# Performance work log

Hardware: AMD Instinct MI355X
Metric: run time of the kernel (lower is better)

The kernel has to match this reference:

```python
import jax, jax.numpy as jnp
import numpy as np

D_CLAMP = 10.0
FAPE_EPS = 1e-4
Z = 10.0
TORSION_EPS = 1e-8


def backbone_fape(R_pred, t_pred, x_pred, R_true, t_true, x_true):
    # R_*: [B,N,3,3], t_*/x_*: [B,N,3]
    Rp_inv = jnp.swapaxes(R_pred, -1, -2)
    tp_inv = -jnp.einsum('birc,bic->bir', Rp_inv, t_pred)
    Rt_inv = jnp.swapaxes(R_true, -1, -2)
    tt_inv = -jnp.einsum('birc,bic->bir', Rt_inv, t_true)
    # [B,N,N,3] local-frame coordinates
    xf_pred = jnp.einsum('biop,bjp->bijo', Rp_inv, x_pred) + tp_inv[:, :, None, :]
    xf_true = jnp.einsum('biop,bjp->bijo', Rt_inv, x_true) + tt_inv[:, :, None, :]
    dist = jnp.sqrt(jnp.sum((xf_pred - xf_true) ** 2, axis=-1) + FAPE_EPS)
    dist = jnp.minimum(dist, D_CLAMP)
    return jnp.mean(dist, axis=(-1, -2)) / Z  # [B]


def torsion_angle_loss(pred, true, true_alt):
    # pred/true/true_alt: [B,N,7,2]
    norm = jnp.sqrt(jnp.sum(pred ** 2, axis=-1, keepdims=True) + TORSION_EPS)
    pred_n = pred / norm
    d_true = jnp.sqrt(jnp.sum((true - pred_n) ** 2, axis=-1, keepdims=True) + TORSION_EPS)
    d_alt = jnp.sqrt(jnp.sum((true_alt - pred_n) ** 2, axis=-1, keepdims=True) + TORSION_EPS)
    torsion = jnp.mean(jnp.minimum(d_true, d_alt), axis=(2, 3))  # [B,N]
    angle_norm = jnp.mean(jnp.abs(norm - 1.0), axis=(2, 3))      # [B,N]
    return torsion + 0.02 * angle_norm


def setup_inputs() -> dict:
    key = jax.random.key(0)
    ks = jax.random.split(key, 7)
    L, B, N = 8, 2, 2048
    return {
        'traj_rotations': jax.random.normal(ks[0], (L, B, N, 3, 3), jnp.float32),
        'traj_translations': jax.random.normal(ks[1], (L, B, N, 3), jnp.float32),
        'traj_torsions': jax.random.normal(ks[2], (L, B, N, 7, 2), jnp.float32),
        'true_rotations': jax.random.normal(ks[3], (B, N, 3, 3), jnp.float32),
        'true_translations': jax.random.normal(ks[4], (B, N, 3), jnp.float32),
        'true_torsion_angles': jax.random.normal(ks[5], (B, N, 7, 2), jnp.float32),
        'true_torsion_angles_alt': jax.random.normal(ks[6], (B, N, 7, 2), jnp.float32),
    }


def reference(traj_rotations, traj_translations, traj_torsions,
              true_rotations, true_translations,
              true_torsion_angles, true_torsion_angles_alt):
    num_layers = traj_rotations.shape[0]
    total = jnp.zeros(traj_rotations.shape[1], traj_rotations.dtype)
    for l in range(num_layers):  # small fixed layer count
        fape = backbone_fape(traj_rotations[l], traj_translations[l], traj_translations[l],
                             true_rotations, true_translations, true_translations)
        torsion = torsion_angle_loss(traj_torsions[l], true_torsion_angles,
                                     true_torsion_angles_alt).mean(axis=-1)
        total = total + fape + torsion
    return total / num_layers
```

## Files before the change

kernel.cpp:

```cpp
#include <hip/hip_runtime.h>
#include <math.h>

constexpr int L = 8;
constexpr int B = 2;
constexpr int N = 2048;
constexpr int LB = L * B;
constexpr int ITEMS = LB * N;
constexpr int KF = 32;

constexpr float D_CLAMP2 = 100.0f;
constexpr float FAPE_EPS = 1e-4f;
constexpr float Z_CONST  = 10.0f;
constexpr float TEPS     = 1e-8f;

constexpr int THREADS = 256;
constexpr int JSPLIT  = 4;
constexpr int JCH     = N / JSPLIT;
constexpr int NPASS   = JCH / 128;
constexpr int NIT     = N / 64;
constexpr int FAPE_BLOCKS = LB * NIT * JSPLIT;
constexpr int TORS_PER_BLK = ITEMS / FAPE_BLOCKS;

typedef __attribute__((ext_vector_type(8))) short bf16x8;
typedef __attribute__((ext_vector_type(4))) float f32x4;

__device__ __forceinline__ float fast_sqrtf(float x) {
    return __builtin_amdgcn_sqrtf(x);
}
__device__ __forceinline__ unsigned short f2bf(float x) {
    unsigned u = __float_as_uint(x);
    u += 0x7fffu + ((u >> 16) & 1u);
    return (unsigned short)(u >> 16);
}
__device__ __forceinline__ float bf2f(unsigned short h) {
    return __uint_as_float((unsigned)h << 16);
}

__device__ __forceinline__ float wave_reduce_sum(float v) {
    #pragma unroll
    for (int off = 32; off > 0; off >>= 1)
        v += __shfl_down(v, off, 64);
    return v;
}

__device__ __forceinline__ float block_reduce_sum(float v) {
    __shared__ float s[4];
    v = wave_reduce_sum(v);
    int lane = threadIdx.x & 63;
    int w    = threadIdx.x >> 6;
    __syncthreads();
    if (lane == 0) s[w] = v;
    __syncthreads();
    return s[0] + s[1] + s[2] + s[3];
}

__device__ __forceinline__ void store_row(short* base, int r, const float* f) {
    #pragma unroll
    for (int c = 0; c < 4; ++c) {
        bf16x8 v;
        #pragma unroll
        for (int e = 0; e < 8; ++e) v[e] = (short)f2bf(f[8 * c + e]);
        const int p = c ^ ((r >> 1) & 3);
        *(bf16x8*)(base + r * KF + p * 8) = v;
    }
}
__device__ __forceinline__ bf16x8 load_frag(const short* base, int r, int c) {
    const int p = c ^ ((r >> 1) & 3);
    return *(const bf16x8*)(base + r * KF + p * 8);
}

__global__ __launch_bounds__(THREADS)
void fape_all_kernel(const float* __restrict__ traj_rot,
                     const float* __restrict__ traj_trans,
                     const float* __restrict__ traj_tors,
                     const float* __restrict__ true_rot,
                     const float* __restrict__ true_trans,
                     const float* __restrict__ t_true,
                     const float* __restrict__ t_alt,
                     float* __restrict__ partials)
{
    __shared__ short phiL[JCH * KF];
    __shared__ short psiL[64 * KF];
    __shared__ float tors_s;

    const int bid = blockIdx.x;
    const int jh  = bid & (JSPLIT - 1);
    const int it  = (bid >> 2) & (NIT - 1);
    const int lb  = bid >> 7;
    const int b   = lb & (B - 1);
    const int tid = threadIdx.x;

    const float* tp = traj_trans + (size_t)lb * N * 3;
    const float* tt = true_trans + (size_t)b  * N * 3;

    #pragma unroll
    for (int half = 0; half < 2; ++half) {
        const int r = tid + half * THREADS;
        const int j = jh * JCH + r;
        float u[6] = { tp[3 * j], tp[3 * j + 1], tp[3 * j + 2],
                       tt[3 * j], tt[3 * j + 1], tt[3 * j + 2] };
        float phi[KF];
        #pragma unroll
        for (int c = 0; c < 6; ++c) phi[c] = u[c] * u[c];
        int idx = 6;
        #pragma unroll
        for (int c = 0; c < 6; ++c)
            #pragma unroll
            for (int d = c + 1; d < 6; ++d)
                phi[idx++] = u[c] * u[d];
        #pragma unroll
        for (int c = 0; c < 6; ++c) phi[21 + c] = u[c];
        phi[27] = 1.0f;
        phi[28] = 1.0f;
        phi[29] = phi[30] = phi[31] = 0.0f;
        store_row(phiL, r, phi);
    }

    if (tid < 64) {
        const int r = tid;
        const int i = it * 64 + r;
        const float* Rp = traj_rot + ((size_t)lb * N + i) * 9;
        const float* Rt = true_rot + ((size_t)(b * N + i)) * 9;

        float W0[6], W1[6], W2[6];
        #pragma unroll
        for (int c = 0; c < 3; ++c) {
            W0[c] = Rp[3 * c];      W1[c] = Rp[3 * c + 1];      W2[c] = Rp[3 * c + 2];
            W0[c + 3] = -Rt[3 * c]; W1[c + 3] = -Rt[3 * c + 1]; W2[c + 3] = -Rt[3 * c + 2];
        }
        float u[6] = { tp[3 * i], tp[3 * i + 1], tp[3 * i + 2],
                       tt[3 * i], tt[3 * i + 1], tt[3 * i + 2] };

        float k0 = 0.f, k1 = 0.f, k2 = 0.f;
        #pragma unroll
        for (int c = 0; c < 6; ++c) {
            k0 = fmaf(W0[c], u[c], k0);
            k1 = fmaf(W1[c], u[c], k1);
            k2 = fmaf(W2[c], u[c], k2);
        }
        k0 = -k0; k1 = -k1; k2 = -k2;

        float psi[KF];
        #pragma unroll
        for (int c = 0; c < 6; ++c)
            psi[c] = fmaf(W0[c], W0[c], fmaf(W1[c], W1[c], W2[c] * W2[c]));
        int idx = 6;
        #pragma unroll
        for (int c = 0; c < 6; ++c)
            #pragma unroll
            for (int d = c + 1; d < 6; ++d)
                psi[idx++] = 2.0f * fmaf(W0[c], W0[d], fmaf(W1[c], W1[d], W2[c] * W2[d]));
        #pragma unroll
        for (int c = 0; c < 6; ++c)
            psi[21 + c] = 2.0f * fmaf(W0[c], k0, fmaf(W1[c], k1, W2[c] * k2));
        psi[27] = fmaf(k0, k0, fmaf(k1, k1, fmaf(k2, k2, FAPE_EPS)));
        psi[28] = psi[27] - bf2f(f2bf(psi[27]));
        psi[29] = psi[30] = psi[31] = 0.0f;
        store_row(psiL, r, psi);
    } else if (tid < 128) {
        const int t = tid - 64;
        float val = 0.0f;
        if (t < TORS_PER_BLK) {
            const int g  = bid * TORS_PER_BLK + t;
            const int n  = g & (N - 1);
            const int bn = b * N + n;
            const float* p  = traj_tors + (size_t)g * 14;
            const float* tr = t_true + (size_t)bn * 14;
            const float* al = t_alt  + (size_t)bn * 14;

            float st = 0.0f, sa = 0.0f;
            #pragma unroll
            for (int k = 0; k < 7; ++k) {
                const float px = p[2 * k], py = p[2 * k + 1];
                const float nrm = fast_sqrtf(fmaf(px, px, fmaf(py, py, TEPS)));
                const float inv = __builtin_amdgcn_rcpf(nrm);
                const float pnx = px * inv, pny = py * inv;
                const float tx = tr[2 * k] - pnx, ty = tr[2 * k + 1] - pny;
                const float ax = al[2 * k] - pnx, ay = al[2 * k + 1] - pny;
                const float dt = fast_sqrtf(fmaf(tx, tx, fmaf(ty, ty, TEPS)));
                const float da = fast_sqrtf(fmaf(ax, ax, fmaf(ay, ay, TEPS)));
                st += fminf(dt, da);
                sa += fabsf(nrm - 1.0f);
            }
            val = (st + 0.02f * sa) * (1.0f / 7.0f);
        }
        val = wave_reduce_sum(val);
        if (tid == 64) tors_s = val;
    }

    __syncthreads();

    const int w    = tid >> 6;
    const int lane = tid & 63;
    const int wm   = w >> 1;
    const int wn   = w & 1;
    const int r15  = lane & 15;
    const int cch  = lane >> 4;

    const bf16x8 a0 = load_frag(psiL, wm * 32 + r15, cch);
    const bf16x8 a1 = load_frag(psiL, wm * 32 + 16 + r15, cch);

    const f32x4 z = { 0.f, 0.f, 0.f, 0.f };
    float acc0 = 0.f, acc1 = 0.f, acc2 = 0.f, acc3 = 0.f;

    #pragma unroll
    for (int jp = 0; jp < NPASS; ++jp) {
        const int rb = jp * 128 + wn * 64 + r15;
        const bf16x8 b0 = load_frag(phiL, rb,      cch);
        const bf16x8 b1 = load_frag(phiL, rb + 16, cch);
        const bf16x8 b2 = load_frag(phiL, rb + 32, cch);
        const bf16x8 b3 = load_frag(phiL, rb + 48, cch);

        f32x4 d0 = __builtin_amdgcn_mfma_f32_16x16x32_bf16(a0, b0, z, 0, 0, 0);
        f32x4 d1 = __builtin_amdgcn_mfma_f32_16x16x32_bf16(a0, b1, z, 0, 0, 0);
        f32x4 d2 = __builtin_amdgcn_mfma_f32_16x16x32_bf16(a0, b2, z, 0, 0, 0);
        f32x4 d3 = __builtin_amdgcn_mfma_f32_16x16x32_bf16(a0, b3, z, 0, 0, 0);
        f32x4 d4 = __builtin_amdgcn_mfma_f32_16x16x32_bf16(a1, b0, z, 0, 0, 0);
        f32x4 d5 = __builtin_amdgcn_mfma_f32_16x16x32_bf16(a1, b1, z, 0, 0, 0);
        f32x4 d6 = __builtin_amdgcn_mfma_f32_16x16x32_bf16(a1, b2, z, 0, 0, 0);
        f32x4 d7 = __builtin_amdgcn_mfma_f32_16x16x32_bf16(a1, b3, z, 0, 0, 0);

        #pragma unroll
        for (int e = 0; e < 4; ++e) {
            acc0 += fast_sqrtf(__builtin_amdgcn_fmed3f(d0[e], 0.f, D_CLAMP2));
            acc1 += fast_sqrtf(__builtin_amdgcn_fmed3f(d1[e], 0.f, D_CLAMP2));
            acc2 += fast_sqrtf(__builtin_amdgcn_fmed3f(d2[e], 0.f, D_CLAMP2));
            acc3 += fast_sqrtf(__builtin_amdgcn_fmed3f(d3[e], 0.f, D_CLAMP2));
            acc0 += fast_sqrtf(__builtin_amdgcn_fmed3f(d4[e], 0.f, D_CLAMP2));
            acc1 += fast_sqrtf(__builtin_amdgcn_fmed3f(d5[e], 0.f, D_CLAMP2));
            acc2 += fast_sqrtf(__builtin_amdgcn_fmed3f(d6[e], 0.f, D_CLAMP2));
            acc3 += fast_sqrtf(__builtin_amdgcn_fmed3f(d7[e], 0.f, D_CLAMP2));
        }
    }

    const float tot = block_reduce_sum((acc0 + acc1) + (acc2 + acc3));
    if (tid == 0) {
        const float inv_pairs = 1.0f / ((float)N * (float)N * Z_CONST);
        partials[bid] = tot * inv_pairs + tors_s * (1.0f / (float)N);
    }
}

__global__ __launch_bounds__(THREADS)
void finalize_kernel(const float* __restrict__ partials,
                     float* __restrict__ out)
{
    float fs0 = 0.0f, fs1 = 0.0f;
    for (int t = threadIdx.x; t < FAPE_BLOCKS; t += THREADS) {
        const float v = partials[t];
        if ((t >> 7) & 1) fs1 += v; else fs0 += v;
    }
    const float F0 = block_reduce_sum(fs0);
    const float F1 = block_reduce_sum(fs1);
    if (threadIdx.x == 0) {
        out[0] = F0 / (float)L;
        out[1] = F1 / (float)L;
    }
}

extern "C" void kernel_launch(void* const* d_in, const int* in_sizes, int n_in,
                              void* d_out, int out_size, void* d_ws, size_t ws_size,
                              hipStream_t stream)
{
    const float* traj_rot   = (const float*)d_in[0];
    const float* traj_trans = (const float*)d_in[1];
    const float* traj_tors  = (const float*)d_in[2];
    const float* true_rot   = (const float*)d_in[3];
    const float* true_trans = (const float*)d_in[4];
    const float* true_ta    = (const float*)d_in[5];
    const float* true_taa   = (const float*)d_in[6];

    float* out      = (float*)d_out;
    float* partials = (float*)d_ws;

    fape_all_kernel<<<FAPE_BLOCKS, THREADS, 0, stream>>>(
        traj_rot, traj_trans, traj_tors, true_rot, true_trans,
        true_ta, true_taa, partials);
    finalize_kernel<<<1, THREADS, 0, stream>>>(partials, out);
}
```

Before: 23.70 us.

## Enlarge i-tile to 256 rows per block and use packed bf16 conversion

Result: faster. 20.61 us (-13.0%).

```diff
diff --git a/kernel.cpp b/kernel.cpp
--- a/kernel.cpp
+++ b/kernel.cpp
@@ -5,7 +5,6 @@
 constexpr int B = 2;
 constexpr int N = 2048;
 constexpr int LB = L * B;
-constexpr int ITEMS = LB * N;
 constexpr int KF = 32;
 
 constexpr float D_CLAMP2 = 100.0f;
@@ -14,12 +13,13 @@
 constexpr float TEPS     = 1e-8f;
 
 constexpr int THREADS = 256;
-constexpr int JSPLIT  = 4;
-constexpr int JCH     = N / JSPLIT;
-constexpr int NPASS   = JCH / 128;
-constexpr int NIT     = N / 64;
-constexpr int FAPE_BLOCKS = LB * NIT * JSPLIT;
-constexpr int TORS_PER_BLK = ITEMS / FAPE_BLOCKS;
+constexpr int IBLK    = 256;
+constexpr int JCH     = 512;
+constexpr int NIT     = N / IBLK;
+constexpr int JSPLIT  = N / JCH;
+constexpr int BLK_PER_LB  = NIT * JSPLIT;
+constexpr int FAPE_BLOCKS = LB * BLK_PER_LB;
+constexpr int TORS_PER_BLK = N / BLK_PER_LB;
 
 typedef __attribute__((ext_vector_type(8))) short bf16x8;
 typedef __attribute__((ext_vector_type(4))) float f32x4;
@@ -27,10 +27,10 @@
 __device__ __forceinline__ float fast_sqrtf(float x) {
     return __builtin_amdgcn_sqrtf(x);
 }
-__device__ __forceinline__ unsigned short f2bf(float x) {
-    unsigned u = __float_as_uint(x);
-    u += 0x7fffu + ((u >> 16) & 1u);
-    return (unsigned short)(u >> 16);
+__device__ __forceinline__ unsigned cvt_pk(float lo, float hi) {
+    unsigned r;
+    asm("v_cvt_pk_bf16_f32 %0, %1, %2" : "=v"(r) : "v"(lo), "v"(hi));
+    return r;
 }
 __device__ __forceinline__ float bf2f(unsigned short h) {
     return __uint_as_float((unsigned)h << 16);
@@ -57,11 +57,12 @@
 __device__ __forceinline__ void store_row(short* base, int r, const float* f) {
     #pragma unroll
     for (int c = 0; c < 4; ++c) {
-        bf16x8 v;
-        #pragma unroll
-        for (int e = 0; e < 8; ++e) v[e] = (short)f2bf(f[8 * c + e]);
+        union { unsigned u[4]; bf16x8 v; } q;
+        #pragma unroll
+        for (int e = 0; e < 4; ++e)
+            q.u[e] = cvt_pk(f[8 * c + 2 * e], f[8 * c + 2 * e + 1]);
         const int p = c ^ ((r >> 1) & 3);
-        *(bf16x8*)(base + r * KF + p * 8) = v;
+        *(bf16x8*)(base + r * KF + p * 8) = q.v;
     }
 }
 __device__ __forceinline__ bf16x8 load_frag(const short* base, int r, int c) {
@@ -80,13 +81,13 @@
                      float* __restrict__ partials)
 {
     __shared__ short phiL[JCH * KF];
-    __shared__ short psiL[64 * KF];
+    __shared__ short psiL[IBLK * KF];
     __shared__ float tors_s;
 
     const int bid = blockIdx.x;
     const int jh  = bid & (JSPLIT - 1);
     const int it  = (bid >> 2) & (NIT - 1);
-    const int lb  = bid >> 7;
+    const int lb  = bid >> 5;
     const int b   = lb & (B - 1);
     const int tid = threadIdx.x;
 
@@ -116,9 +117,9 @@
         store_row(phiL, r, phi);
     }
 
-    if (tid < 64) {
+    {
         const int r = tid;
-        const int i = it * 64 + r;
+        const int i = it * IBLK + r;
         const float* Rp = traj_rot + ((size_t)lb * N + i) * 9;
         const float* Rt = true_rot + ((size_t)(b * N + i)) * 9;
 
@@ -154,38 +155,36 @@
         for (int c = 0; c < 6; ++c)
             psi[21 + c] = 2.0f * fmaf(W0[c], k0, fmaf(W1[c], k1, W2[c] * k2));
         psi[27] = fmaf(k0, k0, fmaf(k1, k1, fmaf(k2, k2, FAPE_EPS)));
-        psi[28] = psi[27] - bf2f(f2bf(psi[27]));
+        psi[28] = psi[27] - bf2f((unsigned short)(cvt_pk(psi[27], psi[27]) & 0xffffu));
         psi[29] = psi[30] = psi[31] = 0.0f;
         store_row(psiL, r, psi);
-    } else if (tid < 128) {
-        const int t = tid - 64;
-        float val = 0.0f;
-        if (t < TORS_PER_BLK) {
-            const int g  = bid * TORS_PER_BLK + t;
-            const int n  = g & (N - 1);
-            const int bn = b * N + n;
-            const float* p  = traj_tors + (size_t)g * 14;
-            const float* tr = t_true + (size_t)bn * 14;
-            const float* al = t_alt  + (size_t)bn * 14;
-
-            float st = 0.0f, sa = 0.0f;
-            #pragma unroll
-            for (int k = 0; k < 7; ++k) {
-                const float px = p[2 * k], py = p[2 * k + 1];
-                const float nrm = fast_sqrtf(fmaf(px, px, fmaf(py, py, TEPS)));
-                const float inv = __builtin_amdgcn_rcpf(nrm);
-                const float pnx = px * inv, pny = py * inv;
-                const float tx = tr[2 * k] - pnx, ty = tr[2 * k + 1] - pny;
-                const float ax = al[2 * k] - pnx, ay = al[2 * k + 1] - pny;
-                const float dt = fast_sqrtf(fmaf(tx, tx, fmaf(ty, ty, TEPS)));
-                const float da = fast_sqrtf(fmaf(ax, ax, fmaf(ay, ay, TEPS)));
-                st += fminf(dt, da);
-                sa += fabsf(nrm - 1.0f);
-            }
-            val = (st + 0.02f * sa) * (1.0f / 7.0f);
-        }
+    }
+
+    if (tid < 64) {
+        const int g  = lb * N + (bid & 31) * TORS_PER_BLK + tid;
+        const int n  = g & (N - 1);
+        const int bn = b * N + n;
+        const float* p  = traj_tors + (size_t)g * 14;
+        const float* tr = t_true + (size_t)bn * 14;
+        const float* al = t_alt  + (size_t)bn * 14;
+
+        float st = 0.0f, sa = 0.0f;
+        #pragma unroll
+        for (int k = 0; k < 7; ++k) {
+            const float px = p[2 * k], py = p[2 * k + 1];
+            const float nrm = fast_sqrtf(fmaf(px, px, fmaf(py, py, TEPS)));
+            const float inv = __builtin_amdgcn_rcpf(nrm);
+            const float pnx = px * inv, pny = py * inv;
+            const float tx = tr[2 * k] - pnx, ty = tr[2 * k + 1] - pny;
+            const float ax = al[2 * k] - pnx, ay = al[2 * k + 1] - pny;
+            const float dt = fast_sqrtf(fmaf(tx, tx, fmaf(ty, ty, TEPS)));
+            const float da = fast_sqrtf(fmaf(ax, ax, fmaf(ay, ay, TEPS)));
+            st += fminf(dt, da);
+            sa += fabsf(nrm - 1.0f);
+        }
+        float val = (st + 0.02f * sa) * (1.0f / 7.0f);
         val = wave_reduce_sum(val);
-        if (tid == 64) tors_s = val;
+        if (tid == 0) tors_s = val;
     }
 
     __syncthreads();
@@ -197,39 +196,31 @@
     const int r15  = lane & 15;
     const int cch  = lane >> 4;
 
-    const bf16x8 a0 = load_frag(psiL, wm * 32 + r15, cch);
-    const bf16x8 a1 = load_frag(psiL, wm * 32 + 16 + r15, cch);
+    bf16x8 a[8];
+    #pragma unroll
+    for (int s = 0; s < 8; ++s)
+        a[s] = load_frag(psiL, wm * 128 + s * 16 + r15, cch);
 
     const f32x4 z = { 0.f, 0.f, 0.f, 0.f };
     float acc0 = 0.f, acc1 = 0.f, acc2 = 0.f, acc3 = 0.f;
 
     #pragma unroll
-    for (int jp = 0; jp < NPASS; ++jp) {
-        const int rb = jp * 128 + wn * 64 + r15;
-        const bf16x8 b0 = load_frag(phiL, rb,      cch);
-        const bf16x8 b1 = load_frag(phiL, rb + 16, cch);
-        const bf16x8 b2 = load_frag(phiL, rb + 32, cch);
-        const bf16x8 b3 = load_frag(phiL, rb + 48, cch);
-
-        f32x4 d0 = __builtin_amdgcn_mfma_f32_16x16x32_bf16(a0, b0, z, 0, 0, 0);
-        f32x4 d1 = __builtin_amdgcn_mfma_f32_16x16x32_bf16(a0, b1, z, 0, 0, 0);
-        f32x4 d2 = __builtin_amdgcn_mfma_f32_16x16x32_bf16(a0, b2, z, 0, 0, 0);
-        f32x4 d3 = __builtin_amdgcn_mfma_f32_16x16x32_bf16(a0, b3, z, 0, 0, 0);
-        f32x4 d4 = __builtin_amdgcn_mfma_f32_16x16x32_bf16(a1, b0, z, 0, 0, 0);
-        f32x4 d5 = __builtin_amdgcn_mfma_f32_16x16x32_bf16(a1, b1, z, 0, 0, 0);
-        f32x4 d6 = __builtin_amdgcn_mfma_f32_16x16x32_bf16(a1, b2, z, 0, 0, 0);
-        f32x4 d7 = __builtin_amdgcn_mfma_f32_16x16x32_bf16(a1, b3, z, 0, 0, 0);
-
-        #pragma unroll
-        for (int e = 0; e < 4; ++e) {
-            acc0 += fast_sqrtf(__builtin_amdgcn_fmed3f(d0[e], 0.f, D_CLAMP2));
-            acc1 += fast_sqrtf(__builtin_amdgcn_fmed3f(d1[e], 0.f, D_CLAMP2));
-            acc2 += fast_sqrtf(__builtin_amdgcn_fmed3f(d2[e], 0.f, D_CLAMP2));
-            acc3 += fast_sqrtf(__builtin_amdgcn_fmed3f(d3[e], 0.f, D_CLAMP2));
-            acc0 += fast_sqrtf(__builtin_amdgcn_fmed3f(d4[e], 0.f, D_CLAMP2));
-            acc1 += fast_sqrtf(__builtin_amdgcn_fmed3f(d5[e], 0.f, D_CLAMP2));
-            acc2 += fast_sqrtf(__builtin_amdgcn_fmed3f(d6[e], 0.f, D_CLAMP2));
-            acc3 += fast_sqrtf(__builtin_amdgcn_fmed3f(d7[e], 0.f, D_CLAMP2));
+    for (int jp = 0; jp < 4; ++jp) {
+        const int rb = wn * 256 + jp * 64 + r15;
+        #pragma unroll
+        for (int q = 0; q < 4; ++q) {
+            const bf16x8 bq = load_frag(phiL, rb + q * 16, cch);
+            f32x4 d[8];
+            #pragma unroll
+            for (int s = 0; s < 8; ++s)
+                d[s] = __builtin_amdgcn_mfma_f32_16x16x32_bf16(a[s], bq, z, 0, 0, 0);
+            #pragma unroll
+            for (int s = 0; s < 8; ++s) {
+                acc0 += fast_sqrtf(__builtin_amdgcn_fmed3f(d[s][0], 0.f, D_CLAMP2));
+                acc1 += fast_sqrtf(__builtin_amdgcn_fmed3f(d[s][1], 0.f, D_CLAMP2));
+                acc2 += fast_sqrtf(__builtin_amdgcn_fmed3f(d[s][2], 0.f, D_CLAMP2));
+                acc3 += fast_sqrtf(__builtin_amdgcn_fmed3f(d[s][3], 0.f, D_CLAMP2));
+            }
         }
     }
 
@@ -247,7 +238,7 @@
     float fs0 = 0.0f, fs1 = 0.0f;
     for (int t = threadIdx.x; t < FAPE_BLOCKS; t += THREADS) {
         const float v = partials[t];
-        if ((t >> 7) & 1) fs1 += v; else fs0 += v;
+        if ((t >> 5) & 1) fs1 += v; else fs0 += v;
     }
     const float F0 = block_reduce_sum(fs0);
     const float F1 = block_reduce_sum(fs1);
```
